# Kernel optimization log

Hardware: AMD Instinct MI355X
Metric: run time of the kernel (lower is better)

Reference implementation:

```python
import math
import jax, jax.numpy as jnp
import numpy as np

# ---------------- static config ----------------
L_MAX = 3
DIM = (L_MAX + 1) ** 2            # 16 = dim of 0e+1o+2e+3o
N_NODES = 8000
N_EDGES = 128000                  # avg 16 neighbors / node
F = 32                            # num_features (irrep multiplicity)
S = 10                            # num_species
NB = 8                            # num bessel basis fns
HID = 64                          # radial MLP hidden width
RD_HID = 16                       # readout MLP hidden (16x0e)
R_MAX = 5.0
AVG_NEIGH = 16.0
MEAN, STD = -1.5, 2.0
E0 = -10.0                        # atomic energy offset per node

_f = math.factorial

def _sl(l):
    return slice(l * l, (l + 1) * (l + 1))

# ---------------- real Clebsch-Gordan / Wigner-3j tables ----------------
def _su2_cg(j1, j2, j3):
    C = np.zeros((2 * j1 + 1, 2 * j2 + 1, 2 * j3 + 1))
    for m1 in range(-j1, j1 + 1):
        for m2 in range(-j2, j2 + 1):
            m3 = m1 + m2
            if abs(m3) > j3:
                continue
            pref = (2 * j3 + 1) * _f(j3 + j1 - j2) * _f(j3 - j1 + j2) * _f(j1 + j2 - j3) / _f(j1 + j2 + j3 + 1)
            pref *= _f(j3 + m3) * _f(j3 - m3) * _f(j1 - m1) * _f(j1 + m1) * _f(j2 - m2) * _f(j2 + m2)
            pref = math.sqrt(pref)
            s = 0.0
            for k in range(max(0, j2 - j3 - m1, j1 - j3 + m2), min(j1 + j2 - j3, j1 - m1, j2 + m2) + 1):
                s += (-1) ** k / (_f(k) * _f(j1 + j2 - j3 - k) * _f(j1 - m1 - k) * _f(j2 + m2 - k) * _f(j3 - j2 + m1 + k) * _f(j3 - j1 - m2 + k))
            C[j1 + m1, j2 + m2, j3 + m3] = pref * s
    return C

def _q_r2c(l):
    # complex <- real spherical-harmonic change of basis (e3nn convention)
    q = np.zeros((2 * l + 1, 2 * l + 1), dtype=complex)
    for m in range(-l, 0):
        q[l + m, l + abs(m)] = 1 / math.sqrt(2)
        q[l + m, l - abs(m)] = -1j / math.sqrt(2)
    q[l, l] = 1.0
    for m in range(1, l + 1):
        q[l + m, l + abs(m)] = (-1) ** m / math.sqrt(2)
        q[l + m, l - abs(m)] = 1j * (-1) ** m / math.sqrt(2)
    return (-1j) ** l * q

def _w3j(l1, l2, l3):
    C = _su2_cg(l1, l2, l3).astype(complex)
    C = np.einsum('abc,ai,bj,ck->ijk', C, _q_r2c(l1), _q_r2c(l2), np.conj(_q_r2c(l3)))
    assert np.abs(C.imag).max() < 1e-8
    return np.real(C)

PATHS = [(l1, l2, l3) for l1 in range(L_MAX + 1) for l2 in range(L_MAX + 1)
         for l3 in range(L_MAX + 1) if abs(l1 - l2) <= l3 <= l1 + l2]
NP_PATHS = len(PATHS)  # 34 CG paths
_W3J_NP = {p: _w3j(*p) for p in PATHS}
W3J = {p: jnp.asarray(v, dtype=jnp.float32) for p, v in _W3J_NP.items()}

def _sh_scales():
    # constants making recursively-built SH component-normalized (|Y_l|^2 = 2l+1)
    v = np.array([0.2, -0.6, 0.7]); v = v / np.linalg.norm(v)
    ys = {1: math.sqrt(3.0) * v}
    sc = {}
    for l in range(2, L_MAX + 1):
        t = np.einsum('abc,a,b->c', _W3J_NP[(l - 1, 1, l)], ys[l - 1], ys[1])
        sc[l] = math.sqrt(2 * l + 1) / np.linalg.norm(t)
        ys[l] = sc[l] * t
    return sc
SH_SCALE = _sh_scales()

# ---------------- equivariant building blocks ----------------
def spherical_harmonics(vectors):
    r = jnp.linalg.norm(vectors, axis=-1, keepdims=True)
    u = vectors / jnp.maximum(r, 1e-9)
    y1 = math.sqrt(3.0) * u
    Y = jnp.concatenate([jnp.ones_like(u[:, :1]), y1], axis=-1)
    prev = y1
    for l in range(2, L_MAX + 1):
        cur = SH_SCALE[l] * jnp.einsum('abc,ea,eb->ec', W3J[(l - 1, 1, l)], prev, y1)
        Y = jnp.concatenate([Y, cur], axis=-1)
        prev = cur
    return Y  # [E, 16]

def radial_embedding(r):
    # Bessel basis * polynomial envelope (RadialEmbeddingBlock)
    x = r / R_MAX
    n = jnp.arange(1, NB + 1, dtype=r.dtype)
    b = math.sqrt(2.0 / R_MAX) * jnp.sin(jnp.pi * x[:, None] * n[None, :]) / jnp.maximum(r, 1e-9)[:, None]
    p = 5.0
    env = 1 - (p + 1) * (p + 2) / 2 * x ** p + p * (p + 2) * x ** (p + 1) - p * (p + 1) / 2 * x ** (p + 2)
    env = jnp.where(x < 1.0, env, 0.0)
    return b * env[:, None]  # [E, NB]

def _lin(x, w):
    # e3nn Linear: per-l channel mixing. x [N,F,DIM], w [L_MAX+1,F,F]
    return jnp.concatenate([jnp.einsum('nfa,fg->nga', x[:, :, _sl(l)], w[l]) for l in range(L_MAX + 1)], axis=-1)

def _tp_edge(xs, Y, rw):
    # radially-weighted CG tensor product of node feats with edge SH (InteractionBlock core)
    out = jnp.zeros_like(xs)
    for p, (l1, l2, l3) in enumerate(PATHS):
        t = jnp.einsum('abc,efa,eb->efc', W3J[(l1, l2, l3)], xs[:, :, _sl(l1)], Y[:, _sl(l2)])
        out = out.at[:, :, _sl(l3)].add(rw[:, p, :, None] * t)
    return out

def _tp_node(x, y):
    # channel-wise symmetric CG product (EquivariantProductBasisBlock contraction)
    out = jnp.zeros_like(x)
    for (l1, l2, l3) in PATHS:
        t = jnp.einsum('abc,nfa,nfb->nfc', W3J[(l1, l2, l3)], x[:, :, _sl(l1)], y[:, :, _sl(l2)])
        out = out.at[:, :, _sl(l3)].add(t / math.sqrt(2 * l3 + 1))
    return out

# ---------------- inputs ----------------
def setup_inputs() -> dict:
    key = jax.random.key(0)
    ks = iter(jax.random.split(key, 40))
    def nrm(shape, fan):
        return jax.random.normal(next(ks), shape, dtype=jnp.float32) / math.sqrt(fan)
    inp = {}
    inp['vectors'] = jax.random.normal(next(ks), (N_EDGES, 3), dtype=jnp.float32) * 1.5
    inp['node_z'] = jax.random.randint(next(ks), (N_NODES,), 0, S)
    inp['senders'] = jax.random.randint(next(ks), (N_EDGES,), 0, N_NODES)
    inp['receivers'] = jax.random.randint(next(ks), (N_EDGES,), 0, N_NODES)
    inp['embed'] = nrm((S, F), 1)
    for i in (0, 1):
        inp['r%d_w0' % i] = nrm((NB, HID), NB)
        inp['r%d_w1' % i] = nrm((HID, HID), HID)
        inp['r%d_w2' % i] = nrm((HID, NP_PATHS * F), HID)
        inp['up%d' % i] = nrm((L_MAX + 1, F, F), F)
        inp['post%d' % i] = nrm((L_MAX + 1, F, F), F)
        inp['pb%d' % i] = nrm((S, 3, F), 1)
        inp['pblin%d' % i] = nrm((L_MAX + 1, F, F), F)
    inp['sel0'] = nrm((S, L_MAX + 1, F, F), F)
    inp['ro0'] = nrm((F, 1), F)
    inp['res1'] = nrm((S, F, F), F)
    inp['ro1_a'] = nrm((F, RD_HID), F)
    inp['ro1_b'] = nrm((RD_HID, 1), RD_HID)
    return inp

# ---------------- forward ----------------
def reference(vectors, node_z, senders, receivers, embed,
              r0_w0, r0_w1, r0_w2, up0, post0, pb0, pblin0, sel0, ro0,
              r1_w0, r1_w1, r1_w2, up1, post1, pb1, pblin1, res1, ro1_a, ro1_b):
    N = node_z.shape[0]
    r = jnp.linalg.norm(vectors, axis=-1)
    Y = spherical_harmonics(vectors)
    rad = radial_embedding(r)
    # node embedding: scalars only
    feats = jnp.zeros((N, F, DIM), vectors.dtype).at[:, :, 0].set(embed[node_z])

    def interaction(feats, w0, w1, w2, wup, wpost):
        h = _lin(feats, wup)
        rw = (jax.nn.silu(jax.nn.silu(rad @ w0) @ w1) @ w2).reshape(-1, NP_PATHS, F)
        msgs = _tp_edge(h[senders], Y, rw)
        agg = jax.ops.segment_sum(msgs, receivers, num_segments=N) / AVG_NEIGH
        return _lin(agg, wpost)

    def product_basis(A, wpb, wlin, z):
        B2 = _tp_node(A, A)           # correlation order 2
        B3 = _tp_node(B2, A)          # correlation order 3
        w = wpb[z]                     # [N,3,F] per-species contraction weights
        out = w[:, 0, :, None] * A + w[:, 1, :, None] * B2 + w[:, 2, :, None] * B3
        return _lin(out, wlin)

    # ---- layer 0: selector tensor product, linear readout ----
    h = interaction(feats, r0_w0, r0_w1, r0_w2, up0, post0)
    wz = sel0[node_z]  # FullyConnectedTensorProduct with one-hot species == per-species linear
    h = jnp.concatenate([jnp.einsum('nfa,nfg->nga', h[:, :, _sl(l)], wz[:, l]) for l in range(L_MAX + 1)], axis=-1)
    feats = product_basis(h, pb0, pblin0, node_z)
    e0 = (feats[:, :, 0] @ ro0)[:, 0]

    # ---- layer 1 (last): residual to scalars, nonlinear readout ----
    resid = jnp.einsum('nf,nfg->ng', feats[:, :, 0], res1[node_z])
    h = interaction(feats, r1_w0, r1_w1, r1_w2, up1, post1)
    h = product_basis(h, pb1, pblin1, node_z)
    sc = h[:, :, 0] + resid  # last-layer target irreps = F x 0e
    e1 = (jax.nn.silu(sc @ ro1_a) @ ro1_b)[:, 0]

    node_energies = MEAN + STD * (e0 + e1) + E0
    return jnp.sum(node_energies)
```

## Files before the change

### kernel.cpp

```cpp
#include <hip/hip_runtime.h>
#include <math.h>

#define NF 32
#define NPATHS 34

typedef __attribute__((ext_vector_type(8))) short bf16x8;
typedef __attribute__((ext_vector_type(4))) float f32x4;
typedef __attribute__((ext_vector_type(2))) float f32x2;

__device__ __forceinline__ unsigned short f2bf(float v){
  unsigned u = __float_as_uint(v);
  u += 0x7fffu + ((u>>16)&1u);
  return (unsigned short)(u>>16);
}
__device__ __forceinline__ float bf2f(unsigned short h){
  return __uint_as_float(((unsigned)h)<<16);
}

struct PathTab { int l1[NPATHS]; int l2[NPATHS]; int l3[NPATHS]; };
constexpr PathTab mkpaths(){
  PathTab t{}; int n=0;
  for(int a=0;a<=3;a++)for(int b=0;b<=3;b++)for(int c=0;c<=3;c++){
    int lo = a>b ? a-b : b-a;
    if(c>=lo && c<=a+b){ t.l1[n]=a; t.l2[n]=b; t.l3[n]=c; n++; }
// ... 39 lines not shown
  else { double s = ((r-l)&1)? -1.0:1.0;
         if (col==r) re=s*is2; else if (col==2*l-r) im=s*is2; }
  ccd v{re,im};
  switch(l&3){
    case 1: return ccd{ v.y, -v.x };
    case 2: return ccd{-v.x, -v.y };
    case 3: return ccd{-v.y,  v.x };
    default: return v;
  }
}

constexpr double w3entry(int l1,int l2,int l3,int i,int j,int k){
  double re=0.0;
  for(int a=0;a<2*l1+1;a++){
    ccd qa=cqval(l1,a,i); if(qa.x==0.0&&qa.y==0.0) continue;
    for(int b=0;b<2*l2+1;b++){
      ccd qb=cqval(l2,b,j); if(qb.x==0.0&&qb.y==0.0) continue;
      int m1=a-l1, m2=b-l2, m3=m1+m2;
      if(m3<-l3||m3>l3) continue;
      int c=m3+l3;
      double cg=su2cg(l1,l2,l3,m1,m2); if(cg==0.0) continue;
      ccd qc=cqval(l3,c,k); qc.y=-qc.y;
      if(qc.x==0.0&&qc.y==0.0) continue;
      ccd ab{qa.x*qb.x-qa.y*qb.y, qa.x*qb.y+qa.y*qb.x};
      re += cg*(ab.x*qc.x - ab.y*qc.y);
    }
  }
  return re;
}

template<int L1,int L2,int L3> struct W3Arr { float v[(2*L1+1)*(2*L2+1)*(2*L3+1)]; };
template<int L1,int L2,int L3> constexpr W3Arr<L1,L2,L3> mkW3(double scale){
  W3Arr<L1,L2,L3> r{};
  for(int i=0;i<2*L1+1;i++)
    for(int j=0;j<2*L2+1;j++)
      for(int k=0;k<2*L3+1;k++)
        r.v[(i*(2*L2+1)+j)*(2*L3+1)+k] = (float)(w3entry(L1,L2,L3,i,j,k)*scale);
  return r;
}
template<int L1,int L2,int L3> constexpr W3Arr<L1,L2,L3> W3V = mkW3<L1,L2,L3>(1.0);
template<int L1,int L2,int L3> constexpr W3Arr<L1,L2,L3> W3N = mkW3<L1,L2,L3>(1.0/csqrt(2.0*L3+1.0));

struct SCt { double sc2, sc3; };
constexpr SCt mksc(){
  double v0=0.2,v1=-0.6,v2=0.7;
  double nv=csqrt(v0*v0+v1*v1+v2*v2);
  double s3=csqrt(3.0);
  double y1[3]={s3*v0/nv, s3*v1/nv, s3*v2/nv};
  double t2[5]={0,0,0,0,0}; double n2=0.0;
  for(int c=0;c<5;c++){
    double s=0.0;
    for(int a=0;a<3;a++)for(int b=0;b<3;b++) s += w3entry(1,1,2,a,b,c)*y1[a]*y1[b];
    t2[c]=s; n2+=s*s;
  }
  double sc2=csqrt(5.0)/csqrt(n2);
  double y2[5]={sc2*t2[0],sc2*t2[1],sc2*t2[2],sc2*t2[3],sc2*t2[4]};
  double n3=0.0;
  for(int c=0;c<7;c++){
    double s=0.0;
    for(int a=0;a<5;a++)for(int b=0;b<3;b++) s += w3entry(2,1,3,a,b,c)*y2[a]*y1[b];
    n3+=s*s;
  }
  double sc3=csqrt(7.0)/csqrt(n3);
  return SCt{sc2,sc3};
}
constexpr SCt SCV = mksc();

template<bool NORM,int l1,int l2,int l3,int A,int B,int C>
__device__ __forceinline__ void w3term(const float* __restrict__ x, const float* __restrict__ y,
                                       float rv, float* __restrict__ acc){
  constexpr float w = NORM ? W3N<l1,l2,l3>.v[(A*(2*l2+1)+B)*(2*l3+1)+C]
                           : W3V<l1,l2,l3>.v[(A*(2*l2+1)+B)*(2*l3+1)+C];
  if constexpr (w!=0.0f)
    acc[l3*l3+C] = fmaf(w, x[l1*l1+A]*y[l2*l2+B]*rv, acc[l3*l3+C]);
}
template<bool NORM,int l1,int l2,int l3,int A,int B,int C>
__device__ __forceinline__ void w3loopC(const float* x,const float* y,float rv,float* acc){
  if constexpr (C<2*l3+1){
    w3term<NORM,l1,l2,l3,A,B,C>(x,y,rv,acc);
    w3loopC<NORM,l1,l2,l3,A,B,C+1>(x,y,rv,acc);
  }
}
template<bool NORM,int l1,int l2,int l3,int A,int B>
__device__ __forceinline__ void w3loopB(const float* x,const float* y,float rv,float* acc){
  if constexpr (B<2*l2+1){
    w3loopC<NORM,l1,l2,l3,A,B,0>(x,y,rv,acc);
    w3loopB<NORM,l1,l2,l3,A,B+1>(x,y,rv,acc);
  }
}
template<bool NORM,int l1,int l2,int l3,int A>
__device__ __forceinline__ void w3loopA(const float* x,const float* y,float rv,float* acc){
  if constexpr (A<2*l1+1){
    w3loopB<NORM,l1,l2,l3,A,0>(x,y,rv,acc);
    w3loopA<NORM,l1,l2,l3,A+1>(x,y,rv,acc);
  }
}

template<int P>
__device__ __forceinline__ void tpn_paths(const float* x,const float* y,float* o){
  if constexpr (P<NPATHS){
    constexpr int l1=PT.l1[P], l2=PT.l2[P], l3=PT.l3[P];
    w3loopA<true,l1,l2,l3,0>(x,y,1.0f,o);
    tpn_paths<P+1>(x,y,o);
  }
}

__device__ __forceinline__ float tpn_scalar(const float* x,const float* y){
  float o[1]={0.f};
  w3loopA<true,0,0,0,0>(x,y,1.0f,o);
  w3loopA<true,1,1,0,0>(x,y,1.0f,o);
  w3loopA<true,2,2,0,0>(x,y,1.0f,o);
  w3loopA<true,3,3,0,0>(x,y,1.0f,o);
  return o[0];
}

template<int l1,int l2,int l3,int A,int B>
constexpr bool anyNZ(){
  for(int c=0;c<2*l3+1;c++)
    if(W3V<l1,l2,l3>.v[(A*(2*l2+1)+B)*(2*l3+1)+c]!=0.0f) return true;
  return false;
}
template<int l1,int l2,int l3,int A,int B,int C>
__device__ __forceinline__ void w3C2(const f32x2 p, f32x2* __restrict__ S){
  constexpr float w = W3V<l1,l2,l3>.v[(A*(2*l2+1)+B)*(2*l3+1)+C];
  if constexpr (w!=0.0f) S[C] = p*w + S[C];
  if constexpr (C+1<2*l3+1) w3C2<l1,l2,l3,A,B,C+1>(p,S);
}
template<int l1,int l2,int l3,int A,int B>
__device__ __forceinline__ void w3B2(const f32x2* __restrict__ x,const f32x2* __restrict__ y,
                                     f32x2* __restrict__ S){
  if constexpr (anyNZ<l1,l2,l3,A,B>()){
    f32x2 p = x[l1*l1+A]*y[l2*l2+B];
    w3C2<l1,l2,l3,A,B,0>(p,S);
  }
  if constexpr (B+1<2*l2+1) w3B2<l1,l2,l3,A,B+1>(x,y,S);
}
template<int l1,int l2,int l3,int A>
__device__ __forceinline__ void w3A2(const f32x2* __restrict__ x,const f32x2* __restrict__ y,
                                     f32x2* __restrict__ S){
  w3B2<l1,l2,l3,A,0>(x,y,S);
  if constexpr (A+1<2*l1+1) w3A2<l1,l2,l3,A+1>(x,y,S);
}
template<bool L0,int P>
__device__ __forceinline__ void tp2(const f32x2* __restrict__ x,const f32x2* __restrict__ y,
                                    const unsigned short* __restrict__ rp,
                                    f32x2* __restrict__ acc){
  if constexpr (P<NPATHS){
    constexpr int l1=PT.l1[P], l2=PT.l2[P], l3=PT.l3[P];
    if constexpr (!(L0 && l1!=0)){
      f32x2 S[2*l3+1];
      #pragma unroll
      for(int c=0;c<2*l3+1;c++) S[c]=(f32x2){0.f,0.f};
      w3A2<l1,l2,l3,0>(x,y,S);
      f32x2 rv = { bf2f(rp[P*576]), bf2f(rp[P*576+4]) };
      #pragma unroll
      for(int c=0;c<2*l3+1;c++) acc[l3*l3+c] = rv*S[c] + acc[l3*l3+c];
    }
    tp2<L0,P+1>(x,y,rp,acc);
  }
}

__global__ __launch_bounds__(256) void k_count(
    const int* __restrict__ rcv, int* __restrict__ deg, int E)
{
  int e=blockIdx.x*256+threadIdx.x;
  if(e>=E) return;
  atomicAdd(&deg[rcv[e]],1);
}

#define SCAN_PER 32
__global__ __launch_bounds__(1024) void k_scan(
    const int* __restrict__ deg, int* __restrict__ row,
    int* __restrict__ cur, int N)
{
  __shared__ int part[1024];
  int t=threadIdx.x;
  int per=(N+1023)/1024; if(per>SCAN_PER) per=SCAN_PER;
  int base=t*per;
  int loc[SCAN_PER];
  int s=0;
  for(int i=0;i<per;i++){ int idx=base+i; int v=(idx<N)? deg[idx]:0; loc[i]=s; s+=v; }
  part[t]=s;
  __syncthreads();
  for(int off=1;off<1024;off<<=1){
    int v=(t>=off)? part[t-off]:0;
    __syncthreads();
    part[t]+=v;
    __syncthreads();
  }
  int ex=(t==0)?0:part[t-1];
  for(int i=0;i<per;i++){
    int idx=base+i;
    if(idx<N){ int r=ex+loc[i]; row[idx]=r; cur[idx]=r; }
  }
  if(t==1023) row[N]=part[1023];
}

__global__ __launch_bounds__(256) void k_fill(
    const int* __restrict__ rcv, int* __restrict__ cur,
    int* __restrict__ eid, int E)
{
  int e=blockIdx.x*256+threadIdx.x;
  if(e>=E) return;
  int pos=atomicAdd(&cur[rcv[e]],1);
  eid[pos]=e;
}

__global__ __launch_bounds__(256) void k_edge_setup(
    const float* __restrict__ vec, const int* __restrict__ snd,
    const int* __restrict__ rcv, const int* __restrict__ eid,
    float* __restrict__ Y, float* __restrict__ rad,
    int* __restrict__ snd_s, int* __restrict__ rcv_s, int E)
{
  int j = blockIdx.x*256+threadIdx.x;
  if (j>=E) return;
  int e = eid[j];
  snd_s[j]=snd[e];
  rcv_s[j]=rcv[e];
  float vx=vec[3*e], vy=vec[3*e+1], vz=vec[3*e+2];
  float r=sqrtf(vx*vx+vy*vy+vz*vz);
  float inv=1.0f/fmaxf(r,1e-9f);
  float y[16];
  y[0]=1.0f;
  const float s3=1.7320508075688772f;
  y[1]=s3*vx*inv; y[2]=s3*vy*inv; y[3]=s3*vz*inv;
  constexpr float sc2=(float)SCV.sc2, sc3=(float)SCV.sc3;
  {
    float t[16];
    #pragma unroll
    for(int c=0;c<16;c++) t[c]=0.f;
    w3loopA<false,1,1,2,0>(y,y,1.0f,t);
    #pragma unroll
    for(int c=0;c<5;c++) y[4+c]=sc2*t[4+c];
    w3loopA<false,2,1,3,0>(y,y,1.0f,t);
    #pragma unroll
    for(int c=0;c<7;c++) y[9+c]=sc3*t[9+c];
  }
  float4* Yp=(float4*)(Y+(size_t)j*16);
  Yp[0]=make_float4(y[0],y[1],y[2],y[3]);
  Yp[1]=make_float4(y[4],y[5],y[6],y[7]);
  Yp[2]=make_float4(y[8],y[9],y[10],y[11]);
  Yp[3]=make_float4(y[12],y[13],y[14],y[15]);
  float x = r*0.2f;
  float env=0.f;
  if (x<1.0f){
    float x2=x*x; float x4=x2*x2; float x5=x4*x;
    env = 1.0f - 21.0f*x5 + 35.0f*x5*x - 15.0f*x5*x2;
  }
  const float cb = 0.632455532033675866f;
  float base = inv*env*cb;
  #pragma unroll
  for(int n=1;n<=8;n++)
    rad[(size_t)j*8 + n-1] = base*sinf(3.14159265358979323846f * x * (float)n);
}

__global__ __launch_bounds__(256) void k_embed16(
    const float* __restrict__ embed, const float* __restrict__ up0,
    const int* __restrict__ z, unsigned short* __restrict__ hl16, int N)
{
  int t=blockIdx.x*256+threadIdx.x;
  int n=t>>5, g=t&31;
  if(n>=N) return;
  const float* ep=embed+z[n]*32;
  float a=0.f;
  #pragma unroll 8
  for(int f=0;f<32;f++) a=fmaf(ep[f],up0[(f<<5)+g],a);
  bf16x8 o0={(short)f2bf(a),0,0,0,0,0,0,0};
  bf16x8 o1={0,0,0,0,0,0,0,0};
  bf16x8* op=(bf16x8*)(hl16+(size_t)n*512+g*16);
  op[0]=o0; op[1]=o1;
}

__global__ __launch_bounds__(256) void k_radial(
    const float* __restrict__ rad, const float* __restrict__ w0,
    const float* __restrict__ w1, unsigned short* __restrict__ hid, int E)
{
  __shared__ float w0s[8*64];
  __shared__ float w1s[64*64];
  int tid=threadIdx.x;
  for(int i=tid;i<512;i+=256) w0s[i]=w0[i];
  for(int i=tid;i<4096;i+=256) w1s[i]=w1[i];
  __syncthreads();
  int e=blockIdx.x*256+tid;
  if(e>=E) return;
  const float4* rp=(const float4*)(rad+(size_t)e*8);
  float4 ra=rp[0], rb=rp[1];
  float rv[8]={ra.x,ra.y,ra.z,ra.w,rb.x,rb.y,rb.z,rb.w};
  float h1[64];
  #pragma unroll 8
  for(int j=0;j<64;j++){
    float a=0.f;
    #pragma unroll
    for(int i=0;i<8;i++) a=fmaf(rv[i],w0s[i*64+j],a);
    h1[j]=a/(1.f+__expf(-a));
  }
  unsigned short* hp = hid+(size_t)e*64;
  #pragma unroll 4
  for(int j=0;j<64;j++){
    float a=0.f;
    #pragma unroll
    for(int i=0;i<64;i++) a=fmaf(h1[i],w1s[i*64+j],a);
    hp[j]=f2bf(a/(1.f+__expf(-a)));
  }
}

__global__ __launch_bounds__(256) void k_prep(
    const float* __restrict__ w2a, const float* __restrict__ w2b,
    unsigned short* __restrict__ ta, unsigned short* __restrict__ tb,
    const float* __restrict__ post0, const float* __restrict__ sel0,
    float* __restrict__ comb)
{
  int t=blockIdx.x*256+threadIdx.x;
  const int C2=2*1088*64;
  if(t<C2){
    const float* src = (t<1088*64)? w2a : w2b;
    unsigned short* dst = (t<1088*64)? ta : tb;
    int u = (t<1088*64)? t : t-1088*64;
    int c=u>>6, k=u&63;
    dst[(size_t)c*64+k]=f2bf(src[(size_t)k*1088+c]);
  } else {
    int u=t-C2;
    if(u<10*4096){
      int z=u>>12, r=u&4095;
      int l=r>>10, e=(r>>5)&31, g=r&31;
      const float* pp=post0+l*1024+e*32;
      const float* sp=sel0+(size_t)z*4096+l*1024;
      float a=0.f;
      #pragma unroll 8
      for(int f=0;f<32;f++) a=fmaf(pp[f], sp[f*32+g], a);
      comb[(size_t)z*4096 + l*1024 + e*32 + g]=a;
    }
  }
}

template<bool L0>
__global__ __launch_bounds__(256,3) void k_tp_fused(
    const unsigned short* __restrict__ hlin, const float* __restrict__ Y,
    const unsigned short* __restrict__ hid, const unsigned short* __restrict__ w2t,
    const int* __restrict__ snd_s, const int* __restrict__ rcv_s,
    float* __restrict__ agg, int eb, int ecnt)
{
  constexpr int NT  = L0 ? 8 : 68;
  constexpr int PD  = L0 ? 4 : 34;
  constexpr int RWSU = PD*32*18;
  constexpr int LMU  = 8704*2;
  constexpr int LDSU = RWSU > LMU ? RWSU : LMU;
  __shared__ unsigned short rws[LDSU] __attribute__((aligned(16)));
  __shared__ int r16v[16];
  int tid=threadIdx.x;
  int lane=tid&63, wave=tid>>6;
  int m16=lane&15, quad=lane>>4;
  int el0=blockIdx.x*16;
  int f=tid&31;
  int hb=(tid>>5)&1;
  int le_base = wave + hb*8;
  int el_s0 = el0 + le_base;
  int el_s1 = el0 + le_base + 4;
  bool actA = el_s0<ecnt, okB = el_s1<ecnt;
  int s0 = actA ? snd_s[eb+el_s0] : 0;
  int s1 = okB  ? snd_s[eb+el_s1] : 0;
  if(tid<16) r16v[tid] = (el0+tid<ecnt) ? rcv_s[eb+el0+tid] : -1;
  {
    const unsigned short* Ab = hid + (size_t)el0*64;
    bf16x8 a0 = *(const bf16x8*)(Ab + m16*64 + quad*8);
    bf16x8 a1 = *(const bf16x8*)(Ab + m16*64 + 32 + quad*8);
    #pragma unroll 2
    for(int nt=wave; nt<NT; nt+=4){
      int col = nt*16 + m16;
      bf16x8 b0 = *(const bf16x8*)(w2t + (size_t)col*64 + quad*8);
      bf16x8 b1 = *(const bf16x8*)(w2t + (size_t)col*64 + 32 + quad*8);
      f32x4 acc = (f32x4){0.f,0.f,0.f,0.f};
      acc = __builtin_amdgcn_mfma_f32_16x16x32_bf16(a0,b0,acc,0,0,0);
      acc = __builtin_amdgcn_mfma_f32_16x16x32_bf16(a1,b1,acc,0,0,0);
      int fc = col&31, P = col>>5;
      unsigned w0 = (unsigned)f2bf(acc[0]) | ((unsigned)f2bf(acc[1])<<16);
      unsigned w1 = (unsigned)f2bf(acc[2]) | ((unsigned)f2bf(acc[3])<<16);
      unsigned* wp = (unsigned*)(rws + (size_t)(P*32+fc)*18 + quad*4);
      wp[0]=w0; wp[1]=w1;
    }
  }
  __syncthreads();
  size_t jA = actA ? (size_t)(eb+el_s0) : 0;
  size_t jB = okB  ? (size_t)(eb+el_s1) : 0;
  f32x2 hs[16];
  if constexpr (L0){
    hs[0] = (f32x2){ bf2f(hlin[(size_t)s0*512 + f*16]),
                     bf2f(hlin[(size_t)s1*512 + f*16]) };
  } else {
    const bf16x8* hA = (const bf16x8*)(hlin + (size_t)s0*512 + f*16);
    const bf16x8* hB = (const bf16x8*)(hlin + (size_t)s1*512 + f*16);
    bf16x8 ha0=hA[0], ha1=hA[1], hb0=hB[0], hb1=hB[1];
    #pragma unroll
    for(int c=0;c<8;c++){
      hs[c]   = (f32x2){ bf2f((unsigned short)ha0[c]), bf2f((unsigned short)hb0[c]) };
      hs[8+c] = (f32x2){ bf2f((unsigned short)ha1[c]), bf2f((unsigned short)hb1[c]) };
    }
  }
  f32x2 yv[16];
  {
    const float4* yA=(const float4*)(Y+jA*16);
    const float4* yB=(const float4*)(Y+jB*16);
    float4 a0=yA[0],a1=yA[1],a2=yA[2],a3=yA[3];
    float4 b0=yB[0],b1=yB[1],b2=yB[2],b3=yB[3];
    yv[0]=(f32x2){a0.x,b0.x}; yv[1]=(f32x2){a0.y,b0.y}; yv[2]=(f32x2){a0.z,b0.z}; yv[3]=(f32x2){a0.w,b0.w};
    yv[4]=(f32x2){a1.x,b1.x}; yv[5]=(f32x2){a1.y,b1.y}; yv[6]=(f32x2){a1.z,b1.z}; yv[7]=(f32x2){a1.w,b1.w};
    yv[8]=(f32x2){a2.x,b2.x}; yv[9]=(f32x2){a2.y,b2.y}; yv[10]=(f32x2){a2.z,b2.z}; yv[11]=(f32x2){a2.w,b2.w};
    yv[12]=(f32x2){a3.x,b3.x}; yv[13]=(f32x2){a3.y,b3.y}; yv[14]=(f32x2){a3.z,b3.z}; yv[15]=(f32x2){a3.w,b3.w};
  }
  const unsigned short* rp = rws + f*18 + le_base;
  f32x2 acc[16];
  #pragma unroll
  for(int c=0;c<16;c++) acc[c]=(f32x2){0.f,0.f};
  tp2<L0,0>(hs,yv,rp,acc);
  __syncthreads();
  float* lm = (float*)rws;
  if(actA){
    #pragma unroll
    for(int c=0;c<16;c++) lm[(le_base*32+f)*17+c] = acc[c].x*0.0625f;
  }
  if(okB){
    #pragma unroll
    for(int c=0;c<16;c++) lm[((le_base+4)*32+f)*17+c] = acc[c].y*0.0625f;
  }
  __syncthreads();
  #pragma unroll
  for(int s=tid; s<512; s+=256){
    int ff=s>>4, cc=s&15;
    float run=0.f; int cur=-1;
    #pragma unroll
    for(int le=0; le<16; le++){
      int rr = r16v[le];
      if(rr != cur){
        if(cur >= 0) atomicAdd(agg + (size_t)cur*512 + s, run);
        run = 0.f; cur = rr;
      }
      if(rr >= 0) run += lm[(le*32+ff)*17 + cc];
    }
    if(cur >= 0) atomicAdd(agg + (size_t)cur*512 + s, run);
  }
}

__global__ __launch_bounds__(256) void k_node0(
    const float* __restrict__ agg, const float* __restrict__ combw,
    const float* __restrict__ pb0, const float* __restrict__ pblin0,
    const float* __restrict__ ro0, const float* __restrict__ res1,
    const float* __restrict__ up1, const int* __restrict__ z,
    float* __restrict__ e0, float* __restrict__ resid,
    unsigned short* __restrict__ hl16, int N)
{
  __shared__ float sh1[8*512] __attribute__((aligned(16)));
  __shared__ float sh2[8*512] __attribute__((aligned(16)));
  int tid=threadIdx.x;
  int n0=tid>>5, g=tid&31;
  int n=blockIdx.x*8+n0;
  bool act=(n<N);
  int zz = act? z[n] : 0;
  if(act){
    const float* wp = combw + (size_t)zz*4096;
    const float* ip = agg + (size_t)n*512;
    float A[16];
    #pragma unroll
    for(int c=0;c<16;c++) A[c]=0.f;
    #pragma unroll 8
    for(int f=0;f<NF;f++){
      const float4* xp=(const float4*)(ip+f*16);
      float4 x0=xp[0],x1=xp[1],x2=xp[2],x3=xp[3];
      float w0v=wp[(f<<5)+g],w1v=wp[1024+(f<<5)+g],w2v=wp[2048+(f<<5)+g],w3v=wp[3072+(f<<5)+g];
      A[0]=fmaf(x0.x,w0v,A[0]);  A[1]=fmaf(x0.y,w1v,A[1]);  A[2]=fmaf(x0.z,w1v,A[2]);  A[3]=fmaf(x0.w,w1v,A[3]);
      A[4]=fmaf(x1.x,w2v,A[4]);  A[5]=fmaf(x1.y,w2v,A[5]);  A[6]=fmaf(x1.z,w2v,A[6]);  A[7]=fmaf(x1.w,w2v,A[7]);
      A[8]=fmaf(x2.x,w2v,A[8]);  A[9]=fmaf(x2.y,w3v,A[9]);  A[10]=fmaf(x2.z,w3v,A[10]);A[11]=fmaf(x2.w,w3v,A[11]);
      A[12]=fmaf(x3.x,w3v,A[12]);A[13]=fmaf(x3.y,w3v,A[13]);A[14]=fmaf(x3.z,w3v,A[14]);A[15]=fmaf(x3.w,w3v,A[15]);
    }
    float B2[16],B3[16];
    #pragma unroll
    for(int c=0;c<16;c++){ B2[c]=0.f; B3[c]=0.f; }
    tpn_paths<0>(A,A,B2);
    tpn_paths<0>(B2,A,B3);
    float wa=pb0[zz*96+g], wb=pb0[zz*96+32+g], wc=pb0[zz*96+64+g];
    #pragma unroll
    for(int c=0;c<16;c++) sh1[n0*512+g*16+c]=wa*A[c]+wb*B2[c]+wc*B3[c];
  }
  __syncthreads();
  if(act){
    float ft[16];
    #pragma unroll
    for(int c=0;c<16;c++) ft[c]=0.f;
    const float* wp=pblin0;
    #pragma unroll 8
    for(int f=0;f<NF;f++){
      const float4* xp=(const float4*)(sh1+n0*512+f*16);
      float4 x0=xp[0],x1=xp[1],x2=xp[2],x3=xp[3];
      float w0v=wp[(f<<5)+g],w1v=wp[1024+(f<<5)+g],w2v=wp[2048+(f<<5)+g],w3v=wp[3072+(f<<5)+g];
      ft[0]=fmaf(x0.x,w0v,ft[0]);  ft[1]=fmaf(x0.y,w1v,ft[1]);  ft[2]=fmaf(x0.z,w1v,ft[2]);  ft[3]=fmaf(x0.w,w1v,ft[3]);
      ft[4]=fmaf(x1.x,w2v,ft[4]);  ft[5]=fmaf(x1.y,w2v,ft[5]);  ft[6]=fmaf(x1.z,w2v,ft[6]);  ft[7]=fmaf(x1.w,w2v,ft[7]);
      ft[8]=fmaf(x2.x,w2v,ft[8]);  ft[9]=fmaf(x2.y,w3v,ft[9]);  ft[10]=fmaf(x2.z,w3v,ft[10]);ft[11]=fmaf(x2.w,w3v,ft[11]);
      ft[12]=fmaf(x3.x,w3v,ft[12]);ft[13]=fmaf(x3.y,w3v,ft[13]);ft[14]=fmaf(x3.z,w3v,ft[14]);ft[15]=fmaf(x3.w,w3v,ft[15]);
    }
    #pragma unroll
    for(int c=0;c<16;c++) sh2[n0*512+g*16+c]=ft[c];
  }
  __syncthreads();
  if(act){
    const float* wp=res1+(size_t)zz*1024;
    float a=0.f;
    #pragma unroll 8
    for(int f=0;f<32;f++) a=fmaf(sh2[n0*512+f*16], wp[(f<<5)+g], a);
    resid[(size_t)n*32+g]=a;
    if(g==0){
      float b=0.f;
      #pragma unroll 8
      for(int f=0;f<32;f++) b=fmaf(sh2[n0*512+f*16], ro0[f], b);
      e0[n]=b;
    }
    float acc[16];
    #pragma unroll
    for(int c=0;c<16;c++) acc[c]=0.f;
    const float* wp2=up1;
    #pragma unroll 8
    for(int f=0;f<NF;f++){
      const float4* xp=(const float4*)(sh2+n0*512+f*16);
      float4 x0=xp[0],x1=xp[1],x2=xp[2],x3=xp[3];
      float w0v=wp2[(f<<5)+g],w1v=wp2[1024+(f<<5)+g],w2v=wp2[2048+(f<<5)+g],w3v=wp2[3072+(f<<5)+g];
      acc[0]=fmaf(x0.x,w0v,acc[0]);  acc[1]=fmaf(x0.y,w1v,acc[1]);  acc[2]=fmaf(x0.z,w1v,acc[2]);  acc[3]=fmaf(x0.w,w1v,acc[3]);
      acc[4]=fmaf(x1.x,w2v,acc[4]);  acc[5]=fmaf(x1.y,w2v,acc[5]);  acc[6]=fmaf(x1.z,w2v,acc[6]);  acc[7]=fmaf(x1.w,w2v,acc[7]);
      acc[8]=fmaf(x2.x,w2v,acc[8]);  acc[9]=fmaf(x2.y,w3v,acc[9]);  acc[10]=fmaf(x2.z,w3v,acc[10]);acc[11]=fmaf(x2.w,w3v,acc[11]);
      acc[12]=fmaf(x3.x,w3v,acc[12]);acc[13]=fmaf(x3.y,w3v,acc[13]);acc[14]=fmaf(x3.z,w3v,acc[14]);acc[15]=fmaf(x3.w,w3v,acc[15]);
    }
    bf16x8 o0,o1;
    #pragma unroll
    for(int c=0;c<8;c++){ o0[c]=(short)f2bf(acc[c]); o1[c]=(short)f2bf(acc[8+c]); }
    bf16x8* op=(bf16x8*)(hl16+(size_t)n*512+g*16);
    op[0]=o0; op[1]=o1;
  }
}

__global__ __launch_bounds__(256) void k_node1(
    const float* __restrict__ agg, const float* __restrict__ post1,
    const float* __restrict__ pb1, const float* __restrict__ pblin1,
    const int* __restrict__ z, const float* __restrict__ resid,
    const float* __restrict__ e0a, const float* __restrict__ ro1a,
    const float* __restrict__ ro1b, float* __restrict__ out, int N)
{
  __shared__ float sh[8*32];
  __shared__ float sh2[8*32];
  __shared__ float red[8];
  int tid=threadIdx.x;
  int n0=tid>>5, g=tid&31;
  int n=blockIdx.x*8+n0;
  bool act=(n<N);
  if(act){
    const float* wp=post1;
    const float* ip=agg+(size_t)n*512;
    float A[16];
    #pragma unroll
    for(int c=0;c<16;c++) A[c]=0.f;
    #pragma unroll 8
    for(int f=0;f<NF;f++){
      const float4* xp=(const float4*)(ip+f*16);
      float4 x0=xp[0],x1=xp[1],x2=xp[2],x3=xp[3];
      float w0v=wp[(f<<5)+g],w1v=wp[1024+(f<<5)+g],w2v=wp[2048+(f<<5)+g],w3v=wp[3072+(f<<5)+g];
      A[0]=fmaf(x0.x,w0v,A[0]);  A[1]=fmaf(x0.y,w1v,A[1]);  A[2]=fmaf(x0.z,w1v,A[2]);  A[3]=fmaf(x0.w,w1v,A[3]);
      A[4]=fmaf(x1.x,w2v,A[4]);  A[5]=fmaf(x1.y,w2v,A[5]);  A[6]=fmaf(x1.z,w2v,A[6]);  A[7]=fmaf(x1.w,w2v,A[7]);
      A[8]=fmaf(x2.x,w2v,A[8]);  A[9]=fmaf(x2.y,w3v,A[9]);  A[10]=fmaf(x2.z,w3v,A[10]);A[11]=fmaf(x2.w,w3v,A[11]);
      A[12]=fmaf(x3.x,w3v,A[12]);A[13]=fmaf(x3.y,w3v,A[13]);A[14]=fmaf(x3.z,w3v,A[14]);A[15]=fmaf(x3.w,w3v,A[15]);
    }
    float B2[16];
    #pragma unroll
    for(int c=0;c<16;c++) B2[c]=0.f;
    tpn_paths<0>(A,A,B2);
    float B3_0=tpn_scalar(B2,A);
    int zz=z[n];
    float wa=pb1[zz*96+g], wb=pb1[zz*96+32+g], wc=pb1[zz*96+64+g];
    sh[n0*32+g]=wa*A[0]+wb*B2[0]+wc*B3_0;
  }
  __syncthreads();
  if(act){
    float a=0.f;
    #pragma unroll 8
    for(int f=0;f<32;f++) a=fmaf(sh[n0*32+f], pblin1[(f<<5)+g], a);
    sh2[n0*32+g]=a+resid[(size_t)n*32+g];
  }
  __syncthreads();
  if(g==0){
    float val=0.f;
    if(act){
      float e1=0.f;
      #pragma unroll
      for(int j=0;j<16;j++){
        float a=0.f;
        #pragma unroll
        for(int f=0;f<32;f++) a=fmaf(sh2[n0*32+f],ro1a[f*16+j],a);
        float s=a/(1.f+__expf(-a));
        e1=fmaf(s,ro1b[j],e1);
      }
      val=-1.5f+2.0f*(e0a[n]+e1)-10.0f;
    }
    red[n0]=val;
  }
  __syncthreads();
  if(tid==0){
    float s=0.f;
    #pragma unroll
    for(int i=0;i<8;i++) s+=red[i];
    atomicAdd(out,s);
  }
}

extern "C" void kernel_launch(void* const* d_in, const int* in_sizes, int n_in,
                              void* d_out, int out_size, void* d_ws, size_t ws_size,
                              hipStream_t stream)
{
  const float* vec   =(const float*)d_in[0];
  const int*   zarr  =(const int*)  d_in[1];
  const int*   snd   =(const int*)  d_in[2];
  const int*   rcv   =(const int*)  d_in[3];
  const float* embed =(const float*)d_in[4];
  const float* r0w0  =(const float*)d_in[5];
  const float* r0w1  =(const float*)d_in[6];
  const float* r0w2  =(const float*)d_in[7];
  const float* up0   =(const float*)d_in[8];
  const float* post0 =(const float*)d_in[9];
  const float* pb0   =(const float*)d_in[10];
  const float* pblin0=(const float*)d_in[11];
  const float* r1w0  =(const float*)d_in[12];
  const float* r1w1  =(const float*)d_in[13];
  const float* r1w2  =(const float*)d_in[14];
  const float* up1   =(const float*)d_in[15];
  const float* post1 =(const float*)d_in[16];
  const float* pb1   =(const float*)d_in[17];
  const float* pblin1=(const float*)d_in[18];
  const float* sel0  =(const float*)d_in[19];
  const float* ro0   =(const float*)d_in[20];
  const float* res1  =(const float*)d_in[21];
  const float* ro1a  =(const float*)d_in[22];
  const float* ro1b  =(const float*)d_in[23];

  const int E = in_sizes[0]/3;
  const int N = in_sizes[1];
  const int Epad = (E+63)&~63;

  char* ws=(char*)d_ws;
  size_t o=0;
  auto alloc=[&](size_t bytes)->char*{
    char* p=ws+o;
    o=(o+bytes+255)&~(size_t)255;
    return p;
  };
  int*   deg  =(int*)  alloc((size_t)N*4);
  int*   rowp =(int*)  alloc((size_t)(N+1)*4);
  int*   cur  =(int*)  alloc((size_t)N*4);
  int*   eid  =(int*)  alloc((size_t)E*4);
  int*   snd_s=(int*)  alloc((size_t)E*4);
  int*   rcv_s=(int*)  alloc((size_t)E*4);
  float* Yb   =(float*)alloc((size_t)E*16*4);
  float* radb =(float*)alloc((size_t)E*8*4);
  unsigned short* hidb=(unsigned short*)alloc((size_t)(Epad+16)*64*2);
  unsigned short* w2t0=(unsigned short*)alloc((size_t)1088*64*2);
  unsigned short* w2t1=(unsigned short*)alloc((size_t)1088*64*2);
  unsigned short* hl16=(unsigned short*)alloc((size_t)N*512*2);
  float* combw=(float*)alloc((size_t)10*4096*4);
  float* bufB =(float*)alloc((size_t)N*512*4);
  float* bufC =(float*)alloc((size_t)N*512*4);
  float* e0b  =(float*)alloc((size_t)N*4);
  float* residb=(float*)alloc((size_t)N*32*4);

  dim3 tb(256);
  dim3 nblk((unsigned)((N*32+255)/256));
  dim3 n8blk((unsigned)((N+7)/8));
  dim3 eblk((unsigned)((E+255)/256));
  dim3 e16blk((unsigned)((E+15)/16));

  hipMemsetAsync(deg,0,(size_t)N*4,stream);
  k_count<<<eblk,tb,0,stream>>>(rcv,deg,E);
  k_scan<<<dim3(1),dim3(1024),0,stream>>>(deg,rowp,cur,N);
  k_fill<<<eblk,tb,0,stream>>>(rcv,cur,eid,E);

  k_edge_setup<<<eblk,tb,0,stream>>>(vec,snd,rcv,eid,Yb,radb,snd_s,rcv_s,E);
  k_prep<<<dim3((2*1088*64+10*4096+255)/256),tb,0,stream>>>(r0w2,r1w2,w2t0,w2t1,post0,sel0,combw);
  k_embed16<<<nblk,tb,0,stream>>>(embed,up0,zarr,hl16,N);

  auto run_edges=[&](bool l0, const unsigned short* hlin, const unsigned short* w2t, float* agg){
    hipMemsetAsync(agg,0,(size_t)N*512*4,stream);
    if(l0) k_tp_fused<true ><<<e16blk,tb,0,stream>>>(hlin,Yb,hidb,w2t,snd_s,rcv_s,agg,0,E);
    else   k_tp_fused<false><<<e16blk,tb,0,stream>>>(hlin,Yb,hidb,w2t,snd_s,rcv_s,agg,0,E);
  };

  k_radial<<<eblk,tb,0,stream>>>(radb,r0w0,r0w1,hidb,E);
  run_edges(true,hl16,w2t0,bufB);
  k_node0<<<n8blk,tb,0,stream>>>(bufB,combw,pb0,pblin0,ro0,res1,up1,zarr,e0b,residb,hl16,N);

  k_radial<<<eblk,tb,0,stream>>>(radb,r1w0,r1w1,hidb,E);
  run_edges(false,hl16,w2t1,bufC);
  hipMemsetAsync(d_out,0,4,stream);
  k_node1<<<n8blk,tb,0,stream>>>(bufC,post1,pb1,pblin1,zarr,residb,e0b,ro1a,ro1b,(float*)d_out,N);
}
```

Baseline: 582.7 us.

## Fuse radial MLP into edge tensor-product kernel, dropping hidden buffer

Removes the separate k_radial kernel and computes the two-layer radial MLP for each 16-edge tile inside k_tp_fused. Each thread computes 4 hidden units of one edge, staging layer-1 activations in shared memory, and the bf16 layer-2 output goes into a new LDS tile that feeds the MFMA. This removes two kernel launches and the global write and read of the per-edge hidden buffer. In exchange it adds two block barriers, reads the weights from global or cache with no LDS staging, and adds a small amount of LDS that could affect occupancy.

```diff
diff --git a/kernel.cpp b/kernel.cpp
--- a/kernel.cpp
+++ b/kernel.cpp
@@ -332,39 +332,6 @@
   bf16x8 o1={0,0,0,0,0,0,0,0};
   bf16x8* op=(bf16x8*)(hl16+(size_t)n*512+g*16);
   op[0]=o0; op[1]=o1;
-}
-
-__global__ __launch_bounds__(256) void k_radial(
-    const float* __restrict__ rad, const float* __restrict__ w0,
-    const float* __restrict__ w1, unsigned short* __restrict__ hid, int E)
-{
-  __shared__ float w0s[8*64];
-  __shared__ float w1s[64*64];
-  int tid=threadIdx.x;
-  for(int i=tid;i<512;i+=256) w0s[i]=w0[i];
-  for(int i=tid;i<4096;i+=256) w1s[i]=w1[i];
-  __syncthreads();
-  int e=blockIdx.x*256+tid;
-  if(e>=E) return;
-  const float4* rp=(const float4*)(rad+(size_t)e*8);
-  float4 ra=rp[0], rb=rp[1];
-  float rv[8]={ra.x,ra.y,ra.z,ra.w,rb.x,rb.y,rb.z,rb.w};
-  float h1[64];
-  #pragma unroll 8
-  for(int j=0;j<64;j++){
-    float a=0.f;
-    #pragma unroll
-    for(int i=0;i<8;i++) a=fmaf(rv[i],w0s[i*64+j],a);
-    h1[j]=a/(1.f+__expf(-a));
-  }
-  unsigned short* hp = hid+(size_t)e*64;
-  #pragma unroll 4
-  for(int j=0;j<64;j++){
-    float a=0.f;
-    #pragma unroll
-    for(int i=0;i<64;i++) a=fmaf(h1[i],w1s[i*64+j],a);
-    hp[j]=f2bf(a/(1.f+__expf(-a)));
-  }
 }
 
 __global__ __launch_bounds__(256) void k_prep(
@@ -399,9 +366,10 @@
 template<bool L0>
 __global__ __launch_bounds__(256,3) void k_tp_fused(
     const unsigned short* __restrict__ hlin, const float* __restrict__ Y,
-    const unsigned short* __restrict__ hid, const unsigned short* __restrict__ w2t,
+    const float* __restrict__ rad, const float* __restrict__ w0g,
+    const float* __restrict__ w1g, const unsigned short* __restrict__ w2t,
     const int* __restrict__ snd_s, const int* __restrict__ rcv_s,
-    float* __restrict__ agg, int eb, int ecnt)
+    float* __restrict__ agg, int ecnt)
 {
   constexpr int NT  = L0 ? 8 : 68;
   constexpr int PD  = L0 ? 4 : 34;
@@ -409,6 +377,7 @@
   constexpr int LMU  = 8704*2;
   constexpr int LDSU = RWSU > LMU ? RWSU : LMU;
   __shared__ unsigned short rws[LDSU] __attribute__((aligned(16)));
+  __shared__ unsigned short hid_s[16*72] __attribute__((aligned(16)));
   __shared__ int r16v[16];
   int tid=threadIdx.x;
   int lane=tid&63, wave=tid>>6;
@@ -420,13 +389,45 @@
   int el_s0 = el0 + le_base;
   int el_s1 = el0 + le_base + 4;
   bool actA = el_s0<ecnt, okB = el_s1<ecnt;
-  int s0 = actA ? snd_s[eb+el_s0] : 0;
-  int s1 = okB  ? snd_s[eb+el_s1] : 0;
-  if(tid<16) r16v[tid] = (el0+tid<ecnt) ? rcv_s[eb+el0+tid] : -1;
+  int s0 = actA ? snd_s[el_s0] : 0;
+  int s1 = okB  ? snd_s[el_s1] : 0;
+  if(tid<16) r16v[tid] = (el0+tid<ecnt) ? rcv_s[el0+tid] : -1;
   {
-    const unsigned short* Ab = hid + (size_t)el0*64;
-    bf16x8 a0 = *(const bf16x8*)(Ab + m16*64 + quad*8);
-    bf16x8 a1 = *(const bf16x8*)(Ab + m16*64 + 32 + quad*8);
+    int le0i = tid>>4, tj = tid&15, j4 = tj*4;
+    int el = el0 + le0i;
+    float rv[8];
+    if (el < ecnt){
+      const float4* rp4=(const float4*)(rad+(size_t)el*8);
+      float4 ra=rp4[0], rb=rp4[1];
+      rv[0]=ra.x; rv[1]=ra.y; rv[2]=ra.z; rv[3]=ra.w;
+      rv[4]=rb.x; rv[5]=rb.y; rv[6]=rb.z; rv[7]=rb.w;
+    } else {
+      #pragma unroll
+      for(int i=0;i<8;i++) rv[i]=0.f;
+    }
+    float* h1s = (float*)rws;
+    #pragma unroll
+    for(int jj=0;jj<4;jj++){
+      int j=j4+jj;
+      float a=0.f;
+      #pragma unroll
+      for(int i=0;i<8;i++) a=fmaf(rv[i], w0g[i*64+j], a);
+      h1s[le0i*68+j]=a/(1.f+__expf(-a));
+    }
+    __syncthreads();
+    #pragma unroll
+    for(int jj=0;jj<4;jj++){
+      int j=j4+jj;
+      float a=0.f;
+      #pragma unroll 16
+      for(int i=0;i<64;i++) a=fmaf(h1s[le0i*68+i], w1g[i*64+j], a);
+      hid_s[le0i*72+j]=f2bf(a/(1.f+__expf(-a)));
+    }
+    __syncthreads();
+  }
+  {
+    bf16x8 a0 = *(const bf16x8*)(hid_s + m16*72 + quad*8);
+    bf16x8 a1 = *(const bf16x8*)(hid_s + m16*72 + 32 + quad*8);
     #pragma unroll 2
     for(int nt=wave; nt<NT; nt+=4){
       int col = nt*16 + m16;
@@ -443,8 +444,8 @@
     }
   }
   __syncthreads();
-  size_t jA = actA ? (size_t)(eb+el_s0) : 0;
-  size_t jB = okB  ? (size_t)(eb+el_s1) : 0;
+  size_t jA = actA ? (size_t)el_s0 : 0;
+  size_t jB = okB  ? (size_t)el_s1 : 0;
   f32x2 hs[16];
   if constexpr (L0){
     hs[0] = (f32x2){ bf2f(hlin[(size_t)s0*512 + f*16]),
@@ -700,7 +701,6 @@
 
   const int E = in_sizes[0]/3;
   const int N = in_sizes[1];
-  const int Epad = (E+63)&~63;
 
   char* ws=(char*)d_ws;
   size_t o=0;
@@ -717,7 +717,6 @@
   int*   rcv_s=(int*)  alloc((size_t)E*4);
   float* Yb   =(float*)alloc((size_t)E*16*4);
   float* radb =(float*)alloc((size_t)E*8*4);
-  unsigned short* hidb=(unsigned short*)alloc((size_t)(Epad+16)*64*2);
   unsigned short* w2t0=(unsigned short*)alloc((size_t)1088*64*2);
   unsigned short* w2t1=(unsigned short*)alloc((size_t)1088*64*2);
   unsigned short* hl16=(unsigned short*)alloc((size_t)N*512*2);
@@ -742,18 +741,17 @@
   k_prep<<<dim3((2*1088*64+10*4096+255)/256),tb,0,stream>>>(r0w2,r1w2,w2t0,w2t1,post0,sel0,combw);
   k_embed16<<<nblk,tb,0,stream>>>(embed,up0,zarr,hl16,N);
 
-  auto run_edges=[&](bool l0, const unsigned short* hlin, const unsigned short* w2t, float* agg){
+  auto run_edges=[&](bool l0, const unsigned short* hlin, const float* w0,
+                     const float* w1, const unsigned short* w2t, float* agg){
     hipMemsetAsync(agg,0,(size_t)N*512*4,stream);
-    if(l0) k_tp_fused<true ><<<e16blk,tb,0,stream>>>(hlin,Yb,hidb,w2t,snd_s,rcv_s,agg,0,E);
-    else   k_tp_fused<false><<<e16blk,tb,0,stream>>>(hlin,Yb,hidb,w2t,snd_s,rcv_s,agg,0,E);
+    if(l0) k_tp_fused<true ><<<e16blk,tb,0,stream>>>(hlin,Yb,radb,w0,w1,w2t,snd_s,rcv_s,agg,E);
+    else   k_tp_fused<false><<<e16blk,tb,0,stream>>>(hlin,Yb,radb,w0,w1,w2t,snd_s,rcv_s,agg,E);
   };
 
-  k_radial<<<eblk,tb,0,stream>>>(radb,r0w0,r0w1,hidb,E);
-  run_edges(true,hl16,w2t0,bufB);
+  run_edges(true,hl16,r0w0,r0w1,w2t0,bufB);
   k_node0<<<n8blk,tb,0,stream>>>(bufB,combw,pb0,pblin0,ro0,res1,up1,zarr,e0b,residb,hl16,N);
 
-  k_radial<<<eblk,tb,0,stream>>>(radb,r1w0,r1w1,hidb,E);
-  run_edges(false,hl16,w2t1,bufC);
+  run_edges(false,hl16,r1w0,r1w1,w2t1,bufC);
   hipMemsetAsync(d_out,0,4,stream);
   k_node1<<<n8blk,tb,0,stream>>>(bufC,post1,pb1,pblin1,zarr,residb,e0b,ro1a,ro1b,(float*)d_out,N);
 }
```

Result: slower. 1.327 ms (+127.7%).

## Process 32 edges per block in fused tensor-product kernel to reuse radial weights

Applied to the files above, without the earlier changes.

Each block now handles 32 edges instead of 16. The radial-MLP MFMA reuses each loaded w2t B fragment across two 16-edge A groups, and every thread evaluates two edge pairs in sequence. The aim is to halve redundant w2t global loads per edge and to lengthen the segmented reduction runs, which should mean fewer atomics. In exchange each thread holds two 16-wide f32x2 accumulator sets, so register pressure rises; the occupancy hint of 3 in launch bounds is dropped, and the block needs more LDS.

```diff
diff --git a/kernel.cpp b/kernel.cpp
--- a/kernel.cpp
+++ b/kernel.cpp
@@ -215,7 +215,7 @@
       #pragma unroll
       for(int c=0;c<2*l3+1;c++) S[c]=(f32x2){0.f,0.f};
       w3A2<l1,l2,l3,0>(x,y,S);
-      f32x2 rv = { bf2f(rp[P*576]), bf2f(rp[P*576+4]) };
+      f32x2 rv = { bf2f(rp[P*1088]), bf2f(rp[P*1088+16]) };
       #pragma unroll
       for(int c=0;c<2*l3+1;c++) acc[l3*l3+c] = rv*S[c] + acc[l3*l3+c];
     }
@@ -397,107 +397,129 @@
 }
 
 template<bool L0>
-__global__ __launch_bounds__(256,3) void k_tp_fused(
+__global__ __launch_bounds__(256) void k_tp_fused(
     const unsigned short* __restrict__ hlin, const float* __restrict__ Y,
     const unsigned short* __restrict__ hid, const unsigned short* __restrict__ w2t,
     const int* __restrict__ snd_s, const int* __restrict__ rcv_s,
-    float* __restrict__ agg, int eb, int ecnt)
+    float* __restrict__ agg, int ecnt)
 {
   constexpr int NT  = L0 ? 8 : 68;
   constexpr int PD  = L0 ? 4 : 34;
-  constexpr int RWSU = PD*32*18;
-  constexpr int LMU  = 8704*2;
+  constexpr int RWSU = PD*32*34;
+  constexpr int LMU  = 32*32*17*2;
   constexpr int LDSU = RWSU > LMU ? RWSU : LMU;
   __shared__ unsigned short rws[LDSU] __attribute__((aligned(16)));
-  __shared__ int r16v[16];
+  __shared__ int r32v[32];
   int tid=threadIdx.x;
   int lane=tid&63, wave=tid>>6;
   int m16=lane&15, quad=lane>>4;
-  int el0=blockIdx.x*16;
+  int el0=blockIdx.x*32;
   int f=tid&31;
-  int hb=(tid>>5)&1;
-  int le_base = wave + hb*8;
-  int el_s0 = el0 + le_base;
-  int el_s1 = el0 + le_base + 4;
-  bool actA = el_s0<ecnt, okB = el_s1<ecnt;
-  int s0 = actA ? snd_s[eb+el_s0] : 0;
-  int s1 = okB  ? snd_s[eb+el_s1] : 0;
-  if(tid<16) r16v[tid] = (el0+tid<ecnt) ? rcv_s[eb+el0+tid] : -1;
+  int q=tid>>5;
+  if(tid<32) r32v[tid] = (el0+tid<ecnt) ? rcv_s[el0+tid] : -1;
   {
     const unsigned short* Ab = hid + (size_t)el0*64;
-    bf16x8 a0 = *(const bf16x8*)(Ab + m16*64 + quad*8);
-    bf16x8 a1 = *(const bf16x8*)(Ab + m16*64 + 32 + quad*8);
+    bf16x8 a0g0 = *(const bf16x8*)(Ab + m16*64 + quad*8);
+    bf16x8 a1g0 = *(const bf16x8*)(Ab + m16*64 + 32 + quad*8);
+    bf16x8 a0g1 = *(const bf16x8*)(Ab + (16+m16)*64 + quad*8);
+    bf16x8 a1g1 = *(const bf16x8*)(Ab + (16+m16)*64 + 32 + quad*8);
     #pragma unroll 2
     for(int nt=wave; nt<NT; nt+=4){
       int col = nt*16 + m16;
       bf16x8 b0 = *(const bf16x8*)(w2t + (size_t)col*64 + quad*8);
       bf16x8 b1 = *(const bf16x8*)(w2t + (size_t)col*64 + 32 + quad*8);
-      f32x4 acc = (f32x4){0.f,0.f,0.f,0.f};
-      acc = __builtin_amdgcn_mfma_f32_16x16x32_bf16(a0,b0,acc,0,0,0);
-      acc = __builtin_amdgcn_mfma_f32_16x16x32_bf16(a1,b1,acc,0,0,0);
+      f32x4 acc0 = (f32x4){0.f,0.f,0.f,0.f};
+      f32x4 acc1 = (f32x4){0.f,0.f,0.f,0.f};
+      acc0 = __builtin_amdgcn_mfma_f32_16x16x32_bf16(a0g0,b0,acc0,0,0,0);
+      acc0 = __builtin_amdgcn_mfma_f32_16x16x32_bf16(a1g0,b1,acc0,0,0,0);
+      acc1 = __builtin_amdgcn_mfma_f32_16x16x32_bf16(a0g1,b0,acc1,0,0,0);
+      acc1 = __builtin_amdgcn_mfma_f32_16x16x32_bf16(a1g1,b1,acc1,0,0,0);
       int fc = col&31, P = col>>5;
-      unsigned w0 = (unsigned)f2bf(acc[0]) | ((unsigned)f2bf(acc[1])<<16);
-      unsigned w1 = (unsigned)f2bf(acc[2]) | ((unsigned)f2bf(acc[3])<<16);
-      unsigned* wp = (unsigned*)(rws + (size_t)(P*32+fc)*18 + quad*4);
-      wp[0]=w0; wp[1]=w1;
-    }
-  }
-  __syncthreads();
-  size_t jA = actA ? (size_t)(eb+el_s0) : 0;
-  size_t jB = okB  ? (size_t)(eb+el_s1) : 0;
-  f32x2 hs[16];
-  if constexpr (L0){
-    hs[0] = (f32x2){ bf2f(hlin[(size_t)s0*512 + f*16]),
-                     bf2f(hlin[(size_t)s1*512 + f*16]) };
-  } else {
-    const bf16x8* hA = (const bf16x8*)(hlin + (size_t)s0*512 + f*16);
-    const bf16x8* hB = (const bf16x8*)(hlin + (size_t)s1*512 + f*16);
-    bf16x8 ha0=hA[0], ha1=hA[1], hb0=hB[0], hb1=hB[1];
-    #pragma unroll
-    for(int c=0;c<8;c++){
-      hs[c]   = (f32x2){ bf2f((unsigned short)ha0[c]), bf2f((unsigned short)hb0[c]) };
-      hs[8+c] = (f32x2){ bf2f((unsigned short)ha1[c]), bf2f((unsigned short)hb1[c]) };
-    }
-  }
-  f32x2 yv[16];
-  {
-    const float4* yA=(const float4*)(Y+jA*16);
-    const float4* yB=(const float4*)(Y+jB*16);
-    float4 a0=yA[0],a1=yA[1],a2=yA[2],a3=yA[3];
-    float4 b0=yB[0],b1=yB[1],b2=yB[2],b3=yB[3];
-    yv[0]=(f32x2){a0.x,b0.x}; yv[1]=(f32x2){a0.y,b0.y}; yv[2]=(f32x2){a0.z,b0.z}; yv[3]=(f32x2){a0.w,b0.w};
-    yv[4]=(f32x2){a1.x,b1.x}; yv[5]=(f32x2){a1.y,b1.y}; yv[6]=(f32x2){a1.z,b1.z}; yv[7]=(f32x2){a1.w,b1.w};
-    yv[8]=(f32x2){a2.x,b2.x}; yv[9]=(f32x2){a2.y,b2.y}; yv[10]=(f32x2){a2.z,b2.z}; yv[11]=(f32x2){a2.w,b2.w};
-    yv[12]=(f32x2){a3.x,b3.x}; yv[13]=(f32x2){a3.y,b3.y}; yv[14]=(f32x2){a3.z,b3.z}; yv[15]=(f32x2){a3.w,b3.w};
-  }
-  const unsigned short* rp = rws + f*18 + le_base;
-  f32x2 acc[16];
+      unsigned* wp = (unsigned*)(rws + (size_t)(P*32+fc)*34);
+      unsigned w0 = (unsigned)f2bf(acc0[0]) | ((unsigned)f2bf(acc0[1])<<16);
+      unsigned w1 = (unsigned)f2bf(acc0[2]) | ((unsigned)f2bf(acc0[3])<<16);
+      wp[quad*2]   = w0;
+      wp[quad*2+1] = w1;
+      unsigned w2 = (unsigned)f2bf(acc1[0]) | ((unsigned)f2bf(acc1[1])<<16);
+      unsigned w3 = (unsigned)f2bf(acc1[2]) | ((unsigned)f2bf(acc1[3])<<16);
+      wp[8+quad*2]   = w2;
+      wp[8+quad*2+1] = w3;
+    }
+  }
+  __syncthreads();
+  f32x2 accP0[16], accP1[16];
+  bool okA0, okB0, okA1, okB1;
   #pragma unroll
-  for(int c=0;c<16;c++) acc[c]=(f32x2){0.f,0.f};
-  tp2<L0,0>(hs,yv,rp,acc);
+  for(int pp=0;pp<2;pp++){
+    int leA = q + pp*8, leB = leA + 16;
+    int elA = el0 + leA, elB = el0 + leB;
+    bool okA = elA<ecnt, okB = elB<ecnt;
+    if(pp==0){ okA0=okA; okB0=okB; } else { okA1=okA; okB1=okB; }
+    int sA = okA ? snd_s[elA] : 0;
+    int sB = okB ? snd_s[elB] : 0;
+    size_t jA = okA ? (size_t)elA : 0;
+    size_t jB = okB ? (size_t)elB : 0;
+    f32x2 hs[16];
+    if constexpr (L0){
+      hs[0] = (f32x2){ bf2f(hlin[(size_t)sA*512 + f*16]),
+                       bf2f(hlin[(size_t)sB*512 + f*16]) };
+    } else {
+      const bf16x8* hA = (const bf16x8*)(hlin + (size_t)sA*512 + f*16);
+      const bf16x8* hB = (const bf16x8*)(hlin + (size_t)sB*512 + f*16);
+      bf16x8 ha0=hA[0], ha1=hA[1], hb0=hB[0], hb1=hB[1];
+      #pragma unroll
+      for(int c=0;c<8;c++){
+        hs[c]   = (f32x2){ bf2f((unsigned short)ha0[c]), bf2f((unsigned short)hb0[c]) };
+        hs[8+c] = (f32x2){ bf2f((unsigned short)ha1[c]), bf2f((unsigned short)hb1[c]) };
+      }
+    }
+    f32x2 yv[16];
+    {
+      const float4* yA=(const float4*)(Y+jA*16);
+      const float4* yB=(const float4*)(Y+jB*16);
+      float4 a0=yA[0],a1=yA[1],a2=yA[2],a3=yA[3];
+      float4 b0=yB[0],b1=yB[1],b2=yB[2],b3=yB[3];
+      yv[0]=(f32x2){a0.x,b0.x}; yv[1]=(f32x2){a0.y,b0.y}; yv[2]=(f32x2){a0.z,b0.z}; yv[3]=(f32x2){a0.w,b0.w};
+      yv[4]=(f32x2){a1.x,b1.x}; yv[5]=(f32x2){a1.y,b1.y}; yv[6]=(f32x2){a1.z,b1.z}; yv[7]=(f32x2){a1.w,b1.w};
+      yv[8]=(f32x2){a2.x,b2.x}; yv[9]=(f32x2){a2.y,b2.y}; yv[10]=(f32x2){a2.z,b2.z}; yv[11]=(f32x2){a2.w,b2.w};
+      yv[12]=(f32x2){a3.x,b3.x}; yv[13]=(f32x2){a3.y,b3.y}; yv[14]=(f32x2){a3.z,b3.z}; yv[15]=(f32x2){a3.w,b3.w};
+    }
+    const unsigned short* rp = rws + f*34 + leA;
+    f32x2* acc = (pp==0)? accP0 : accP1;
+    #pragma unroll
+    for(int c=0;c<16;c++) acc[c]=(f32x2){0.f,0.f};
+    tp2<L0,0>(hs,yv,rp,acc);
+  }
   __syncthreads();
   float* lm = (float*)rws;
-  if(actA){
-    #pragma unroll
-    for(int c=0;c<16;c++) lm[(le_base*32+f)*17+c] = acc[c].x*0.0625f;
-  }
-  if(okB){
-    #pragma unroll
-    for(int c=0;c<16;c++) lm[((le_base+4)*32+f)*17+c] = acc[c].y*0.0625f;
+  if(okA0){
+    #pragma unroll
+    for(int c=0;c<16;c++) lm[((q)*32+f)*17+c] = accP0[c].x*0.0625f;
+  }
+  if(okB0){
+    #pragma unroll
+    for(int c=0;c<16;c++) lm[((q+16)*32+f)*17+c] = accP0[c].y*0.0625f;
+  }
+  if(okA1){
+    #pragma unroll
+    for(int c=0;c<16;c++) lm[((q+8)*32+f)*17+c] = accP1[c].x*0.0625f;
+  }
+  if(okB1){
+    #pragma unroll
+    for(int c=0;c<16;c++) lm[((q+24)*32+f)*17+c] = accP1[c].y*0.0625f;
   }
   __syncthreads();
   #pragma unroll
   for(int s=tid; s<512; s+=256){
-    int ff=s>>4, cc=s&15;
     float run=0.f; int cur=-1;
     #pragma unroll
-    for(int le=0; le<16; le++){
-      int rr = r16v[le];
+    for(int le=0; le<32; le++){
+      int rr = r32v[le];
       if(rr != cur){
         if(cur >= 0) atomicAdd(agg + (size_t)cur*512 + s, run);
         run = 0.f; cur = rr;
       }
-      if(rr >= 0) run += lm[(le*32+ff)*17 + cc];
+      if(rr >= 0) run += lm[(le*32+(s>>4))*17 + (s&15)];
     }
     if(cur >= 0) atomicAdd(agg + (size_t)cur*512 + s, run);
   }
@@ -717,7 +739,7 @@
   int*   rcv_s=(int*)  alloc((size_t)E*4);
   float* Yb   =(float*)alloc((size_t)E*16*4);
   float* radb =(float*)alloc((size_t)E*8*4);
-  unsigned short* hidb=(unsigned short*)alloc((size_t)(Epad+16)*64*2);
+  unsigned short* hidb=(unsigned short*)alloc((size_t)(Epad+32)*64*2);
   unsigned short* w2t0=(unsigned short*)alloc((size_t)1088*64*2);
   unsigned short* w2t1=(unsigned short*)alloc((size_t)1088*64*2);
   unsigned short* hl16=(unsigned short*)alloc((size_t)N*512*2);
@@ -731,7 +753,7 @@
   dim3 nblk((unsigned)((N*32+255)/256));
   dim3 n8blk((unsigned)((N+7)/8));
   dim3 eblk((unsigned)((E+255)/256));
-  dim3 e16blk((unsigned)((E+15)/16));
+  dim3 e32blk((unsigned)((E+31)/32));
 
   hipMemsetAsync(deg,0,(size_t)N*4,stream);
   k_count<<<eblk,tb,0,stream>>>(rcv,deg,E);
@@ -744,8 +766,8 @@
 
   auto run_edges=[&](bool l0, const unsigned short* hlin, const unsigned short* w2t, float* agg){
     hipMemsetAsync(agg,0,(size_t)N*512*4,stream);
-    if(l0) k_tp_fused<true ><<<e16blk,tb,0,stream>>>(hlin,Yb,hidb,w2t,snd_s,rcv_s,agg,0,E);
-    else   k_tp_fused<false><<<e16blk,tb,0,stream>>>(hlin,Yb,hidb,w2t,snd_s,rcv_s,agg,0,E);
+    if(l0) k_tp_fused<true ><<<e32blk,tb,0,stream>>>(hlin,Yb,hidb,w2t,snd_s,rcv_s,agg,E);
+    else   k_tp_fused<false><<<e32blk,tb,0,stream>>>(hlin,Yb,hidb,w2t,snd_s,rcv_s,agg,E);
   };
 
   k_radial<<<eblk,tb,0,stream>>>(radb,r0w0,r0w1,hidb,E);
```

Result: slower. 607.7 us (+4.3%).
